# Performance work log

Hardware: AMD Instinct MI355X
Metric: run time of the kernel (lower is better)

The kernel has to match this reference:

```python
import jax, jax.numpy as jnp
import numpy as np

PATCH = 32
K_FILT = 4
B, NP, C = 32, 256, 3


def _dct_matrix(n):
    i = np.arange(n)[:, None]
    j = np.arange(n)[None, :]
    scale = np.where(i == 0, np.sqrt(1.0 / n), np.sqrt(2.0 / n))
    m = scale * np.cos((j + 0.5) * np.pi * i / n)
    return jnp.asarray(m, dtype=jnp.float32)


def _bandpass_filters(n, k_filt):
    i = np.arange(n)[:, None]
    j = np.arange(n)[None, :]
    s = i + j  # [n, n]
    ks = np.arange(k_filt)[:, None, None]
    lo = 2.0 * n / k_filt * ks
    hi = 2.0 * n / k_filt * (ks + 1)
    f = ((s >= lo) & (s < hi)).astype(np.float32)  # [K, n, n]
    return jnp.asarray(f)


def setup_inputs() -> dict:
    key = jax.random.key(0)
    x = jax.random.normal(key, (B, NP, C, PATCH, PATCH), dtype=jnp.float32)
    return {
        'x': x,
        'dct_matrix': _dct_matrix(PATCH),
        'bandpass_filters': _bandpass_filters(PATCH, K_FILT),
    }


def reference(x, dct_matrix, bandpass_filters):
    # Batched 2D DCT: D @ patch @ D^T for every (b, n, c) patch.
    dct_coeffs = jnp.einsum('ih,bnchw,jw->bncij', dct_matrix, x, dct_matrix)
    log_abs = jnp.log1p(jnp.abs(dct_coeffs))  # log(|X| + 1)
    # patch_score = sum_k sum_c 2^k * (log_abs[c] * filter_k).sum()
    k_weights = 2.0 ** jnp.arange(bandpass_filters.shape[0], dtype=jnp.float32)
    weight_map = jnp.einsum('k,khw->hw', k_weights, bandpass_filters)  # [H, W]
    patch_grades = jnp.einsum('bnchw,hw->bn', log_abs, weight_map)
    return dct_coeffs, patch_grades
```

## Files before the change

### kernel.cpp

```cpp
#include <hip/hip_runtime.h>

#define PATCH 32
#define NPIX  1024
#define CH    3
#define BLK   192

__global__ __launch_bounds__(BLK) void dct_grade_kernel(
    const float* __restrict__ x,
    const float* __restrict__ dct,
    float* __restrict__ out_coeffs,
    float* __restrict__ out_grades)
{
    __shared__ __align__(16) float Dt[NPIX];
    __shared__ __align__(16) float Xs[CH * NPIX];
    __shared__ __align__(16) float Ts[CH * NPIX];
    __shared__ float partial[3];

    const int tid = threadIdx.x;
    const int bn  = blockIdx.x;

    const float4* xg  = reinterpret_cast<const float4*>(x + (size_t)bn * (CH * NPIX));
    float4*       xs4 = reinterpret_cast<float4*>(Xs);
    #pragma unroll
    for (int k = 0; k < 4; ++k)
        xs4[tid + BLK * k] = xg[tid + BLK * k];

    for (int t = tid; t < 256; t += BLK) {
        int i  = t & 31;
        int h0 = (t >> 5) << 2;
        float4 dv = *reinterpret_cast<const float4*>(dct + i * 32 + h0);
        Dt[(h0 + 0) * 32 + i] = dv.x;
        Dt[(h0 + 1) * 32 + i] = dv.y;
        Dt[(h0 + 2) * 32 + i] = dv.z;
        Dt[(h0 + 3) * 32 + i] = dv.w;
    }
    __syncthreads();

    const int wid   = tid >> 6;
    const int lane  = tid & 63;
    const int i0    = (lane >> 3) << 2;
    const int c0    = (lane & 7) << 2;
    const int cbase = wid * NPIX;

    float acc[4][4];
    #pragma unroll
    for (int a = 0; a < 4; ++a)
        #pragma unroll
        for (int b = 0; b < 4; ++b) acc[a][b] = 0.0f;

    #pragma unroll
    for (int h = 0; h < 32; ++h) {
        float4 dv = *reinterpret_cast<const float4*>(&Dt[h * 32 + i0]);
        float4 xv = *reinterpret_cast<const float4*>(&Xs[cbase + h * 32 + c0]);
        float da[4] = {dv.x, dv.y, dv.z, dv.w};
        float xa[4] = {xv.x, xv.y, xv.z, xv.w};
        #pragma unroll
        for (int ii = 0; ii < 4; ++ii)
            #pragma unroll
            for (int ww = 0; ww < 4; ++ww)
                acc[ii][ww] += da[ii] * xa[ww];
    }
    #pragma unroll
    for (int ww = 0; ww < 4; ++ww) {
        float4 col = make_float4(acc[0][ww], acc[1][ww], acc[2][ww], acc[3][ww]);
        *reinterpret_cast<float4*>(&Ts[cbase + (c0 + ww) * 32 + i0]) = col;
    }
    __syncthreads();

    float y[4][4];
    #pragma unroll
    for (int a = 0; a < 4; ++a)
        #pragma unroll
        for (int b = 0; b < 4; ++b) y[a][b] = 0.0f;

    #pragma unroll
    for (int w = 0; w < 32; ++w) {
        float4 tv = *reinterpret_cast<const float4*>(&Ts[cbase + w * 32 + i0]);
        float4 dv = *reinterpret_cast<const float4*>(&Dt[w * 32 + c0]);
        float ta[4] = {tv.x, tv.y, tv.z, tv.w};
        float da[4] = {dv.x, dv.y, dv.z, dv.w};
        #pragma unroll
        for (int ii = 0; ii < 4; ++ii)
            #pragma unroll
            for (int jj = 0; jj < 4; ++jj)
                y[ii][jj] += ta[ii] * da[jj];
    }

    float* outp = out_coeffs + (size_t)bn * (CH * NPIX) + cbase;
    float g = 0.0f;
    #pragma unroll
    for (int ii = 0; ii < 4; ++ii) {
        int row = i0 + ii;
        float4 st = make_float4(y[ii][0], y[ii][1], y[ii][2], y[ii][3]);
        *reinterpret_cast<float4*>(&outp[row * 32 + c0]) = st;
        #pragma unroll
        for (int jj = 0; jj < 4; ++jj) {
            float wgt = (float)(1 << ((row + c0 + jj) >> 4));
            g += __logf(1.0f + fabsf(y[ii][jj])) * wgt;
        }
    }

    #pragma unroll
    for (int off = 32; off > 0; off >>= 1)
        g += __shfl_down(g, off);
    if (lane == 0) partial[wid] = g;
    __syncthreads();
    if (tid == 0)
        out_grades[bn] = partial[0] + partial[1] + partial[2];
}

extern "C" void kernel_launch(void* const* d_in, const int* in_sizes, int n_in,
                              void* d_out, int out_size, void* d_ws, size_t ws_size,
                              hipStream_t stream) {
    const float* x   = (const float*)d_in[0];
    const float* dct = (const float*)d_in[1];
    float* out_coeffs = (float*)d_out;
    float* out_grades = (float*)d_out + (size_t)8192 * CH * NPIX;

    dct_grade_kernel<<<8192, BLK, 0, stream>>>(x, dct, out_coeffs, out_grades);
}
```

Baseline: 189.9 us.

## Map one patch per wavefront and process channels sequentially in per-wave LDS

Work is remapped from one block per patch with one wave per channel to one wavefront per patch, looping over the three channels. Eight patches share a 512-thread block and a single DCT matrix load. A single per-wave 4KB LDS buffer is reused for both input and intermediate, which removes the block-level barriers after the initial one and the cross-wave grade reduction. The trade-off is less memory-level parallelism per wave, since each wave's channel loads are serialized, in exchange for far fewer DCT-matrix loads per patch and lower LDS footprint.

```diff
diff --git a/kernel.cpp b/kernel.cpp
--- a/kernel.cpp
+++ b/kernel.cpp
@@ -1,33 +1,26 @@
 #include <hip/hip_runtime.h>
 
-#define PATCH 32
-#define NPIX  1024
-#define CH    3
-#define BLK   192
+#define NPIX 1024
+#define CH   3
+#define WPB  8
+#define BLK  (WPB * 64)
 
-__global__ __launch_bounds__(BLK) void dct_grade_kernel(
+__global__ __launch_bounds__(BLK, 8) void dct_grade_kernel(
     const float* __restrict__ x,
     const float* __restrict__ dct,
     float* __restrict__ out_coeffs,
     float* __restrict__ out_grades)
 {
     __shared__ __align__(16) float Dt[NPIX];
-    __shared__ __align__(16) float Xs[CH * NPIX];
-    __shared__ __align__(16) float Ts[CH * NPIX];
-    __shared__ float partial[3];
+    __shared__ __align__(16) float S[WPB][NPIX];
 
-    const int tid = threadIdx.x;
-    const int bn  = blockIdx.x;
+    const int tid  = threadIdx.x;
+    const int wid  = tid >> 6;
+    const int lane = tid & 63;
 
-    const float4* xg  = reinterpret_cast<const float4*>(x + (size_t)bn * (CH * NPIX));
-    float4*       xs4 = reinterpret_cast<float4*>(Xs);
-    #pragma unroll
-    for (int k = 0; k < 4; ++k)
-        xs4[tid + BLK * k] = xg[tid + BLK * k];
-
-    for (int t = tid; t < 256; t += BLK) {
-        int i  = t & 31;
-        int h0 = (t >> 5) << 2;
+    if (tid < 256) {
+        int i  = tid & 31;
+        int h0 = (tid >> 5) << 2;
         float4 dv = *reinterpret_cast<const float4*>(dct + i * 32 + h0);
         Dt[(h0 + 0) * 32 + i] = dv.x;
         Dt[(h0 + 1) * 32 + i] = dv.y;
@@ -36,77 +29,88 @@
     }
     __syncthreads();
 
-    const int wid   = tid >> 6;
-    const int lane  = tid & 63;
-    const int i0    = (lane >> 3) << 2;
-    const int c0    = (lane & 7) << 2;
-    const int cbase = wid * NPIX;
+    const int pn = blockIdx.x * WPB + wid;
+    const int i0 = (lane >> 3) << 2;
+    const int c0 = (lane & 7) << 2;
 
-    float acc[4][4];
-    #pragma unroll
-    for (int a = 0; a < 4; ++a)
+    float* Sw = &S[wid][0];
+    const float* xg   = x          + (size_t)pn * (CH * NPIX);
+    float*       outg = out_coeffs + (size_t)pn * (CH * NPIX);
+
+    const int ssum = i0 + c0;
+    float g = 0.0f;
+
+    for (int c = 0; c < CH; ++c) {
+        {
+            const float4* src = reinterpret_cast<const float4*>(xg + c * NPIX);
+            float4*       dst = reinterpret_cast<float4*>(Sw);
+            #pragma unroll
+            for (int k = 0; k < 4; ++k)
+                dst[lane + 64 * k] = src[lane + 64 * k];
+        }
+
+        float acc[4][4];
         #pragma unroll
-        for (int b = 0; b < 4; ++b) acc[a][b] = 0.0f;
+        for (int a = 0; a < 4; ++a)
+            #pragma unroll
+            for (int b = 0; b < 4; ++b) acc[a][b] = 0.0f;
 
-    #pragma unroll
-    for (int h = 0; h < 32; ++h) {
-        float4 dv = *reinterpret_cast<const float4*>(&Dt[h * 32 + i0]);
-        float4 xv = *reinterpret_cast<const float4*>(&Xs[cbase + h * 32 + c0]);
-        float da[4] = {dv.x, dv.y, dv.z, dv.w};
-        float xa[4] = {xv.x, xv.y, xv.z, xv.w};
         #pragma unroll
-        for (int ii = 0; ii < 4; ++ii)
+        for (int h = 0; h < 32; ++h) {
+            float4 dv = *reinterpret_cast<const float4*>(&Dt[h * 32 + i0]);
+            float4 xv = *reinterpret_cast<const float4*>(&Sw[h * 32 + c0]);
+            float da[4] = {dv.x, dv.y, dv.z, dv.w};
+            float xa[4] = {xv.x, xv.y, xv.z, xv.w};
             #pragma unroll
-            for (int ww = 0; ww < 4; ++ww)
-                acc[ii][ww] += da[ii] * xa[ww];
-    }
-    #pragma unroll
-    for (int ww = 0; ww < 4; ++ww) {
-        float4 col = make_float4(acc[0][ww], acc[1][ww], acc[2][ww], acc[3][ww]);
-        *reinterpret_cast<float4*>(&Ts[cbase + (c0 + ww) * 32 + i0]) = col;
-    }
-    __syncthreads();
+            for (int ii = 0; ii < 4; ++ii)
+                #pragma unroll
+                for (int ww = 0; ww < 4; ++ww)
+                    acc[ii][ww] += da[ii] * xa[ww];
+        }
 
-    float y[4][4];
-    #pragma unroll
-    for (int a = 0; a < 4; ++a)
         #pragma unroll
-        for (int b = 0; b < 4; ++b) y[a][b] = 0.0f;
+        for (int ww = 0; ww < 4; ++ww) {
+            float4 col = make_float4(acc[0][ww], acc[1][ww], acc[2][ww], acc[3][ww]);
+            *reinterpret_cast<float4*>(&Sw[(c0 + ww) * 32 + i0]) = col;
+        }
 
-    #pragma unroll
-    for (int w = 0; w < 32; ++w) {
-        float4 tv = *reinterpret_cast<const float4*>(&Ts[cbase + w * 32 + i0]);
-        float4 dv = *reinterpret_cast<const float4*>(&Dt[w * 32 + c0]);
-        float ta[4] = {tv.x, tv.y, tv.z, tv.w};
-        float da[4] = {dv.x, dv.y, dv.z, dv.w};
+        float y[4][4];
         #pragma unroll
-        for (int ii = 0; ii < 4; ++ii)
+        for (int a = 0; a < 4; ++a)
             #pragma unroll
-            for (int jj = 0; jj < 4; ++jj)
-                y[ii][jj] += ta[ii] * da[jj];
-    }
+            for (int b = 0; b < 4; ++b) y[a][b] = 0.0f;
 
-    float* outp = out_coeffs + (size_t)bn * (CH * NPIX) + cbase;
-    float g = 0.0f;
-    #pragma unroll
-    for (int ii = 0; ii < 4; ++ii) {
-        int row = i0 + ii;
-        float4 st = make_float4(y[ii][0], y[ii][1], y[ii][2], y[ii][3]);
-        *reinterpret_cast<float4*>(&outp[row * 32 + c0]) = st;
         #pragma unroll
-        for (int jj = 0; jj < 4; ++jj) {
-            float wgt = (float)(1 << ((row + c0 + jj) >> 4));
-            g += __logf(1.0f + fabsf(y[ii][jj])) * wgt;
+        for (int w = 0; w < 32; ++w) {
+            float4 tv = *reinterpret_cast<const float4*>(&Sw[w * 32 + i0]);
+            float4 dv = *reinterpret_cast<const float4*>(&Dt[w * 32 + c0]);
+            float ta[4] = {tv.x, tv.y, tv.z, tv.w};
+            float da[4] = {dv.x, dv.y, dv.z, dv.w};
+            #pragma unroll
+            for (int ii = 0; ii < 4; ++ii)
+                #pragma unroll
+                for (int jj = 0; jj < 4; ++jj)
+                    y[ii][jj] += ta[ii] * da[jj];
+        }
+
+        float* outp = outg + c * NPIX;
+        #pragma unroll
+        for (int ii = 0; ii < 4; ++ii) {
+            float4 st = make_float4(y[ii][0], y[ii][1], y[ii][2], y[ii][3]);
+            *reinterpret_cast<float4*>(&outp[(i0 + ii) * 32 + c0]) = st;
+            #pragma unroll
+            for (int jj = 0; jj < 4; ++jj) {
+                float wgt = (float)(1 << ((ssum + ii + jj) >> 4));
+                g += __logf(1.0f + fabsf(y[ii][jj])) * wgt;
+            }
         }
     }
 
     #pragma unroll
     for (int off = 32; off > 0; off >>= 1)
         g += __shfl_down(g, off);
-    if (lane == 0) partial[wid] = g;
-    __syncthreads();
-    if (tid == 0)
-        out_grades[bn] = partial[0] + partial[1] + partial[2];
+    if (lane == 0)
+        out_grades[pn] = g;
 }
 
 extern "C" void kernel_launch(void* const* d_in, const int* in_sizes, int n_in,
@@ -117,5 +121,5 @@
     float* out_coeffs = (float*)d_out;
     float* out_grades = (float*)d_out + (size_t)8192 * CH * NPIX;
 
-    dct_grade_kernel<<<8192, BLK, 0, stream>>>(x, dct, out_coeffs, out_grades);
+    dct_grade_kernel<<<8192 / WPB, BLK, 0, stream>>>(x, dct, out_coeffs, out_grades);
 }
```

Measured after the change: 516.2 us. +171.8%, slower.
